# Optimization experiments

Measured on AMD Instinct MI355X. Metric: run time of the kernel, lower is better.

The kernel has to match this reference:

```python
import jax, jax.numpy as jnp
import numpy as np

UNITS = 2048
RHO = 0.99          # spectral_radius
LEAKY = 1.0         # leaky integration coefficient
INPUT_SCALING = 1.0
BIAS_SCALING = 1.0
B, T, D_IN = 32, 512, 128


def setup_inputs() -> dict:
    key = jax.random.key(0)
    k1, k2, k3 = jax.random.split(key, 3)
    inputs = jax.random.normal(k1, (B, T, D_IN), dtype=jnp.float32)
    h0 = jnp.zeros((B, UNITS), dtype=jnp.float32)
    # original uses deterministic +/-1 signs from pi digits; same structure: sign matrix * scaling
    kernel = jnp.where(jax.random.uniform(k2, (D_IN, UNITS)) >= 0.5, 1.0, -1.0).astype(jnp.float32) * INPUT_SCALING
    bias = jnp.where(jax.random.uniform(k3, (UNITS,)) >= 0.5, 1.0, -1.0).astype(jnp.float32) * BIAS_SCALING
    return {"inputs": inputs, "h0": h0, "kernel": kernel, "bias": bias}


def reference(inputs, h0, kernel, bias):
    # Precompute input projection for all timesteps: [B, T, U]
    u = jnp.einsum("btd,du->btu", inputs, kernel)

    def step(h, u_t):
        # prev @ recurrent_kernel == spectral_radius * cyclic shift of prev
        state_part = RHO * jnp.roll(h, 1, axis=-1)
        h_new = h * (1.0 - LEAKY) + jnp.tanh(u_t + bias + state_part) * LEAKY
        return h_new, h_new

    _, ys = jax.lax.scan(step, h0, jnp.swapaxes(u, 0, 1))  # scan over time
    return jnp.swapaxes(ys, 0, 1)  # [B, T, U]
```

## Files before the change

### kernel.cpp

```cpp
#include <hip/hip_runtime.h>
#include <hip/hip_bf16.h>

#define U_ 2048
#define T_ 512
#define K_ 128
#define B_ 32
#define RHO_ 0.99f
#define CPB 128
#define NTILES 9
#define NSLOTS 10

typedef __attribute__((ext_vector_type(8))) short short8;
typedef __attribute__((ext_vector_type(4))) float f32x4;

__device__ __forceinline__ float fast_tanh(float x) {
  float e = __builtin_amdgcn_exp2f(2.8853900817779268f * x);
  return 1.0f - 2.0f * __builtin_amdgcn_rcpf(e + 1.0f);
}

__device__ __forceinline__ unsigned short bf16_rne(float x) {
  unsigned int u = __float_as_uint(x);
  u += 0x7FFFu + ((u >> 16) & 1u);
  return (unsigned short)(u >> 16);
}

#define GLOAD_LDS16(gsrc, ldst)                                        \
  __builtin_amdgcn_global_load_lds(                                    \
      (const __attribute__((address_space(1))) void*)(gsrc),           \
      (__attribute__((address_space(3))) void*)(ldst), 16, 0, 0)

__global__ __launch_bounds__(256) void convert_a_kernel(
    const float* __restrict__ A, unsigned short* __restrict__ Ab) {
  const int gi = blockIdx.x * 256 + threadIdx.x;
  const int m = gi >> 5;
  const int kq = (gi & 31) << 2;
  const float4 v = *(const float4*)&A[(size_t)m * K_ + kq];
  ushort4 hi, lo;
  hi.x = bf16_rne(v.x); hi.y = bf16_rne(v.y); hi.z = bf16_rne(v.z); hi.w = bf16_rne(v.w);
  lo.x = bf16_rne(v.x - __uint_as_float((unsigned)hi.x << 16));
  lo.y = bf16_rne(v.y - __uint_as_float((unsigned)hi.y << 16));
  lo.z = bf16_rne(v.z - __uint_as_float((unsigned)hi.z << 16));
  lo.w = bf16_rne(v.w - __uint_as_float((unsigned)hi.w << 16));
  *(ushort4*)&Ab[(size_t)m * 256 + kq] = hi;
  *(ushort4*)&Ab[(size_t)m * 256 + 128 + kq] = lo;
}

__global__ __launch_bounds__(256) void convert_w_kernel(
    const float* __restrict__ W, unsigned short* __restrict__ Wbt) {
  const int gi = blockIdx.x * 256 + threadIdx.x;
  const int kq = gi >> 11;
  const int n = gi & 2047;
  const int k = kq << 2;
  ushort4 w;
  w.x = bf16_rne(W[(size_t)(k + 0) * U_ + n]);
  w.y = bf16_rne(W[(size_t)(k + 1) * U_ + n]);
  w.z = bf16_rne(W[(size_t)(k + 2) * U_ + n]);
  w.w = bf16_rne(W[(size_t)(k + 3) * U_ + n]);
  *(ushort4*)&Wbt[(size_t)n * 256 + k] = w;
  *(ushort4*)&Wbt[(size_t)n * 256 + 128 + k] = w;
}

__global__ __launch_bounds__(256, 2) void fused_gemm_scan4_kernel(
    const unsigned short* __restrict__ Ab, const unsigned short* __restrict__ Wbt,
    const float* __restrict__ bias, const float* __restrict__ h0,
    float* __restrict__ out) {
  __shared__ unsigned short Wl[NSLOTS * 2048];
  __shared__ unsigned short Al[2][4096];
  __shared__ float u_lds[2][16 * 146];
  const int tid = threadIdx.x;
  const int id = blockIdx.x + (blockIdx.y << 4);
  const int xcd = id & 7;
  const int wk = id >> 3;
  const int b = (xcd << 2) + (wk >> 4);
  const int bx = wk & 15;
  const int c0 = bx << 7;
  const int cbase = bx << 3;
  const int wave = tid >> 6;
  const int lane = tid & 63;
  const int r = lane & 15;
  const int q = lane >> 4;

  const int wrow = tid >> 4;
  const int wlg  = (tid & 15) ^ (wrow & 7);
  const int arow0 = tid >> 5;
  const int alg0  = (tid & 31) ^ (arow0 & 7);
  const int arow1 = 8 + arow0;
  const int alg1  = (tid & 31) ^ (arow1 & 7);

  const unsigned short* const aBase = Ab + (((size_t)b * T_) << 8);

  GLOAD_LDS16(aBase + (((size_t)arow0) << 8) + (alg0 << 3), &Al[0][tid << 3]);
  GLOAD_LDS16(aBase + (((size_t)arow1) << 8) + (alg1 << 3), &Al[0][(tid + 256) << 3]);
  #pragma unroll
  for (int j = 0; j < NTILES; ++j) {
    const int g = (cbase + j) & 127;
    GLOAD_LDS16(Wbt + (((size_t)((g << 4) + wrow)) << 8) + (wlg << 3),
                &Wl[(j << 11) + (tid << 3)]);
  }
  float bv[3], nbv[3];
  bv[0] = bias[(c0 + (wave << 4) + r) & (U_ - 1)];
  bv[1] = bias[(c0 + ((wave + 4) << 4) + r) & (U_ - 1)];
  bv[2] = (wave == 0) ? bias[(c0 + 128 + r) & (U_ - 1)] : 0.0f;
  float h = 0.0f;
  if (tid < CPB)
    h = h0[((size_t)b << 11) + ((c0 + tid + U_ - 1) & (U_ - 1))];

  __syncthreads();

  for (int it = 0; it < T_ / 16; ++it) {
    const int cur = it & 1;
    const int t0 = it << 4;

    if (it + 1 < T_ / 16) {
      GLOAD_LDS16(aBase + (((size_t)(t0 + 16 + arow0)) << 8) + (alg0 << 3),
                  &Al[cur ^ 1][tid << 3]);
      GLOAD_LDS16(aBase + (((size_t)(t0 + 16 + arow1)) << 8) + (alg1 << 3),
                  &Al[cur ^ 1][(tid + 256) << 3]);
      const int g = (cbase + it + NTILES) & 127;
      GLOAD_LDS16(Wbt + (((size_t)((g << 4) + wrow)) << 8) + (wlg << 3),
                  &Wl[(((it + NTILES) % NSLOTS) << 11) + (tid << 3)]);
      nbv[0] = bias[(c0 + t0 + 16 + (wave << 4) + r) & (U_ - 1)];
      nbv[1] = bias[(c0 + t0 + 16 + ((wave + 4) << 4) + r) & (U_ - 1)];
      if (wave == 0) nbv[2] = bias[(c0 + t0 + 16 + 128 + r) & (U_ - 1)];
    }

    short8 af[8];
    #pragma unroll
    for (int ks = 0; ks < 8; ++ks)
      af[ks] = *(const short8*)&Al[cur][(r << 8) + ((((ks << 2) + q) ^ (r & 7)) << 3)];

    #pragma unroll
    for (int u = 0; u < 3; ++u) {
      const int j = (u < 2) ? (wave + (u << 2)) : 8;
      if (u < 2 || wave == 0) {
        const int slot = (it + j) % NSLOTS;
        short8 bfk[4];
        #pragma unroll
        for (int ks = 0; ks < 4; ++ks)
          bfk[ks] = *(const short8*)&Wl[(slot << 11) + (r << 7) +
                                        ((((ks << 2) + q) ^ (r & 7)) << 3)];
        f32x4 acc = (f32x4){0.f, 0.f, 0.f, 0.f};
        #pragma unroll
        for (int ks = 0; ks < 8; ++ks)
          acc = __builtin_amdgcn_mfma_f32_16x16x32_bf16(af[ks], bfk[ks & 3], acc, 0, 0, 0);
        #pragma unroll
        for (int reg = 0; reg < 4; ++reg)
          u_lds[cur][((q << 2) + reg) * 146 + (j << 4) + r] = acc[reg] + bv[u];
      }
    }

    __syncthreads();

    if (tid < CPB) {
      float uv[16];
      #pragma unroll
      for (int tt = 0; tt < 16; ++tt)
        uv[tt] = u_lds[cur][tt * 146 + tid + tt];
      float* const orow = out + (((size_t)(b * T_ + t0)) << 11);
      #pragma unroll
      for (int tt = 0; tt < 16; ++tt) {
        h = fast_tanh(fmaf(RHO_, h, uv[tt]));
        __builtin_nontemporal_store(
            h, &orow[((size_t)tt << 11) + ((c0 + tid + t0 + tt) & (U_ - 1))]);
      }
    }
    bv[0] = nbv[0]; bv[1] = nbv[1]; bv[2] = nbv[2];
  }
}

__global__ __launch_bounds__(256) void ring_scan_kernel(
    float* __restrict__ buf, const float* __restrict__ h0) {
  const int b = blockIdx.y;
  const int c = (blockIdx.x << 8) + threadIdx.x;
  float* const base = buf + (size_t)b * (T_ * U_);
  float h = h0[((size_t)b << 11) + ((c + U_ - 1) & (U_ - 1))];
  float wA[8], wB[8];
  #pragma unroll
  for (int j = 0; j < 8; ++j)
    wA[j] = base[((size_t)j << 11) + ((c + j) & (U_ - 1))];
  for (int t0 = 0; t0 < T_; t0 += 16) {
    #pragma unroll
    for (int j = 0; j < 8; ++j) {
      const int t = t0 + 8 + j;
      wB[j] = base[((size_t)t << 11) + ((c + t) & (U_ - 1))];
    }
    #pragma unroll
    for (int j = 0; j < 8; ++j) {
      const int t = t0 + j;
      h = fast_tanh(fmaf(RHO_, h, wA[j]));
      base[((size_t)t << 11) + ((c + t) & (U_ - 1))] = h;
    }
    if (t0 + 16 < T_) {
      #pragma unroll
      for (int j = 0; j < 8; ++j) {
        const int t = t0 + 16 + j;
        wA[j] = base[((size_t)t << 11) + ((c + t) & (U_ - 1))];
      }
    }
    #pragma unroll
    for (int j = 0; j < 8; ++j) {
      const int t = t0 + 8 + j;
      h = fast_tanh(fmaf(RHO_, h, wB[j]));
      base[((size_t)t << 11) + ((c + t) & (U_ - 1))] = h;
    }
  }
}

__global__ __launch_bounds__(256, 4) void gemm_bias_kernel(
    const float* __restrict__ A, const float* __restrict__ W,
    const float* __restrict__ bias, float* __restrict__ out) {
  __shared__ float Asf[64][68];
  __shared__ float Bsf[64][64];
  const int tid = threadIdx.x;
  const int m0 = blockIdx.y << 6;
  const int n0 = blockIdx.x << 6;
  const int tx = tid & 15;
  const int ty = tid >> 4;
  float acc[4][4] = {};
  #pragma unroll
  for (int kb = 0; kb < 2; ++kb) {
    if (kb) __syncthreads();
    {
      const int c4 = tid & 15;
      const int r0 = tid >> 4;
      #pragma unroll
      for (int rr = 0; rr < 4; ++rr) {
        const int r = r0 + (rr << 4);
        const float4 v = *(const float4*)(A + (size_t)(m0 + r) * K_ + (kb << 6) + (c4 << 2));
        Asf[(c4 << 2) + 0][r] = v.x;
        Asf[(c4 << 2) + 1][r] = v.y;
        Asf[(c4 << 2) + 2][r] = v.z;
        Asf[(c4 << 2) + 3][r] = v.w;
      }
    }
    {
      const int c4 = tid & 15;
      const int r0 = tid >> 4;
      #pragma unroll
      for (int rr = 0; rr < 4; ++rr) {
        const int k = r0 + (rr << 4);
        *(float4*)&Bsf[k][c4 << 2] =
            *(const float4*)(W + (size_t)((kb << 6) + k) * U_ + n0 + (c4 << 2));
      }
    }
    __syncthreads();
    #pragma unroll 16
    for (int k = 0; k < 64; ++k) {
      const float4 a = *(const float4*)&Asf[k][ty << 2];
      const float4 b = *(const float4*)&Bsf[k][tx << 2];
      acc[0][0] = fmaf(a.x, b.x, acc[0][0]); acc[0][1] = fmaf(a.x, b.y, acc[0][1]);
      acc[0][2] = fmaf(a.x, b.z, acc[0][2]); acc[0][3] = fmaf(a.x, b.w, acc[0][3]);
      acc[1][0] = fmaf(a.y, b.x, acc[1][0]); acc[1][1] = fmaf(a.y, b.y, acc[1][1]);
      acc[1][2] = fmaf(a.y, b.z, acc[1][2]); acc[1][3] = fmaf(a.y, b.w, acc[1][3]);
      acc[2][0] = fmaf(a.z, b.x, acc[2][0]); acc[2][1] = fmaf(a.z, b.y, acc[2][1]);
      acc[2][2] = fmaf(a.z, b.z, acc[2][2]); acc[2][3] = fmaf(a.z, b.w, acc[2][3]);
      acc[3][0] = fmaf(a.w, b.x, acc[3][0]); acc[3][1] = fmaf(a.w, b.y, acc[3][1]);
      acc[3][2] = fmaf(a.w, b.z, acc[3][2]); acc[3][3] = fmaf(a.w, b.w, acc[3][3]);
    }
  }
  const float4 bv = *(const float4*)(bias + n0 + (tx << 2));
  #pragma unroll
  for (int i = 0; i < 4; ++i) {
    float4 o;
    o.x = acc[i][0] + bv.x; o.y = acc[i][1] + bv.y;
    o.z = acc[i][2] + bv.z; o.w = acc[i][3] + bv.w;
    *(float4*)(out + (size_t)(m0 + (ty << 2) + i) * U_ + n0 + (tx << 2)) = o;
  }
}

extern "C" void kernel_launch(void* const* d_in, const int* in_sizes, int n_in,
                              void* d_out, int out_size, void* d_ws, size_t ws_size,
                              hipStream_t stream) {
  const float* A    = (const float*)d_in[0];
  const float* h0   = (const float*)d_in[1];
  const float* W    = (const float*)d_in[2];
  const float* bias = (const float*)d_in[3];
  float* out = (float*)d_out;

  const size_t AB_BYTES = (size_t)B_ * T_ * 256 * 2;
  const size_t WB_BYTES = (size_t)U_ * 256 * 2;
  const size_t NEEDED = AB_BYTES + WB_BYTES;

  if (ws_size >= NEEDED) {
    unsigned short* Ab  = (unsigned short*)d_ws;
    unsigned short* Wbt = (unsigned short*)((char*)d_ws + AB_BYTES);

    convert_a_kernel<<<2048, 256, 0, stream>>>(A, Ab);
    convert_w_kernel<<<256, 256, 0, stream>>>(W, Wbt);
    dim3 fg(U_ / CPB, B_);
    fused_gemm_scan4_kernel<<<fg, 256, 0, stream>>>(Ab, Wbt, bias, h0, out);
  } else {
    dim3 gemm_grid(U_ / 64, (B_ * T_) / 64);
    gemm_bias_kernel<<<gemm_grid, 256, 0, stream>>>(A, W, bias, out);
    dim3 scan_grid(U_ / 256, B_);
    ring_scan_kernel<<<scan_grid, 256, 0, stream>>>(out, h0);
  }
}
```

Measured before the change: 192.7 us.

## Defer output stores by one iteration and move async loads to scan waves

The fused GEMM+scan kernel now buffers the 16 scan outputs in registers and stores them at the start of the next iteration, so the global stores overlap the MFMA work. All async global-to-LDS loads are issued by the first 128 threads, and the ninth-tile MFMA moves from wave 0 to wave 2. Together these spread the load across the waves that also run the scan. The block barrier becomes a hand-written waitcnt with vmcnt(16), so it no longer waits on outstanding stores. The tanh recurrence is also reformulated to fold RHO into the next step's FMA and shorten the serial dependency chain. The custom waitcnt depends on how the compiler orders memory operations and could be fragile.

```diff
diff --git a/kernel.cpp b/kernel.cpp
--- a/kernel.cpp
+++ b/kernel.cpp
@@ -12,11 +12,6 @@
 
 typedef __attribute__((ext_vector_type(8))) short short8;
 typedef __attribute__((ext_vector_type(4))) float f32x4;
-
-__device__ __forceinline__ float fast_tanh(float x) {
-  float e = __builtin_amdgcn_exp2f(2.8853900817779268f * x);
-  return 1.0f - 2.0f * __builtin_amdgcn_rcpf(e + 1.0f);
-}
 
 __device__ __forceinline__ unsigned short bf16_rne(float x) {
   unsigned int u = __float_as_uint(x);
@@ -60,7 +55,7 @@
   *(ushort4*)&Wbt[(size_t)n * 256 + 128 + k] = w;
 }
 
-__global__ __launch_bounds__(256, 2) void fused_gemm_scan4_kernel(
+__global__ __launch_bounds__(256, 2) void fused_gemm_scan5_kernel(
     const unsigned short* __restrict__ Ab, const unsigned short* __restrict__ Wbt,
     const float* __restrict__ bias, const float* __restrict__ h0,
     float* __restrict__ out) {
@@ -80,30 +75,36 @@
   const int r = lane & 15;
   const int q = lane >> 4;
 
-  const int wrow = tid >> 4;
-  const int wlg  = (tid & 15) ^ (wrow & 7);
-  const int arow0 = tid >> 5;
-  const int alg0  = (tid & 31) ^ (arow0 & 7);
-  const int arow1 = 8 + arow0;
-  const int alg1  = (tid & 31) ^ (arow1 & 7);
-
   const unsigned short* const aBase = Ab + (((size_t)b * T_) << 8);
 
-  GLOAD_LDS16(aBase + (((size_t)arow0) << 8) + (alg0 << 3), &Al[0][tid << 3]);
-  GLOAD_LDS16(aBase + (((size_t)arow1) << 8) + (alg1 << 3), &Al[0][(tid + 256) << 3]);
-  #pragma unroll
-  for (int j = 0; j < NTILES; ++j) {
-    const int g = (cbase + j) & 127;
-    GLOAD_LDS16(Wbt + (((size_t)((g << 4) + wrow)) << 8) + (wlg << 3),
-                &Wl[(j << 11) + (tid << 3)]);
+  if (tid < 128) {
+    #pragma unroll
+    for (int k = 0; k < 4; ++k) {
+      const int p = tid + (k << 7);
+      const int row = p >> 5, pg = p & 31;
+      GLOAD_LDS16(aBase + ((size_t)row << 8) + ((pg ^ (row & 7)) << 3),
+                  &Al[0][p << 3]);
+    }
+    #pragma unroll
+    for (int j = 0; j < NTILES; ++j) {
+      const int g = (cbase + j) & 127;
+      #pragma unroll
+      for (int k = 0; k < 2; ++k) {
+        const int p = tid + (k << 7);
+        const int row = p >> 4, pg = p & 15;
+        GLOAD_LDS16(Wbt + ((size_t)((g << 4) + row) << 8) + ((pg ^ (row & 7)) << 3),
+                    &Wl[(j << 11) + (p << 3)]);
+      }
+    }
   }
   float bv[3], nbv[3];
   bv[0] = bias[(c0 + (wave << 4) + r) & (U_ - 1)];
   bv[1] = bias[(c0 + ((wave + 4) << 4) + r) & (U_ - 1)];
-  bv[2] = (wave == 0) ? bias[(c0 + 128 + r) & (U_ - 1)] : 0.0f;
-  float h = 0.0f;
+  bv[2] = (wave == 2) ? bias[(c0 + 128 + r) & (U_ - 1)] : 0.0f;
+  float h_prev = 0.0f;
   if (tid < CPB)
-    h = h0[((size_t)b << 11) + ((c0 + tid + U_ - 1) & (U_ - 1))];
+    h_prev = h0[((size_t)b << 11) + ((c0 + tid + U_ - 1) & (U_ - 1))];
+  float hreg[16];
 
   __syncthreads();
 
@@ -111,17 +112,38 @@
     const int cur = it & 1;
     const int t0 = it << 4;
 
+    if (tid < 128 && it + 1 < T_ / 16) {
+      #pragma unroll
+      for (int k = 0; k < 4; ++k) {
+        const int p = tid + (k << 7);
+        const int row = p >> 5, pg = p & 31;
+        GLOAD_LDS16(aBase + ((size_t)(t0 + 16 + row) << 8) + ((pg ^ (row & 7)) << 3),
+                    &Al[cur ^ 1][p << 3]);
+      }
+      const int g = (cbase + it + NTILES) & 127;
+      const int snew = (it + NTILES) % NSLOTS;
+      #pragma unroll
+      for (int k = 0; k < 2; ++k) {
+        const int p = tid + (k << 7);
+        const int row = p >> 4, pg = p & 15;
+        GLOAD_LDS16(Wbt + ((size_t)((g << 4) + row) << 8) + ((pg ^ (row & 7)) << 3),
+                    &Wl[(snew << 11) + (p << 3)]);
+      }
+    }
     if (it + 1 < T_ / 16) {
-      GLOAD_LDS16(aBase + (((size_t)(t0 + 16 + arow0)) << 8) + (alg0 << 3),
-                  &Al[cur ^ 1][tid << 3]);
-      GLOAD_LDS16(aBase + (((size_t)(t0 + 16 + arow1)) << 8) + (alg1 << 3),
-                  &Al[cur ^ 1][(tid + 256) << 3]);
-      const int g = (cbase + it + NTILES) & 127;
-      GLOAD_LDS16(Wbt + (((size_t)((g << 4) + wrow)) << 8) + (wlg << 3),
-                  &Wl[(((it + NTILES) % NSLOTS) << 11) + (tid << 3)]);
       nbv[0] = bias[(c0 + t0 + 16 + (wave << 4) + r) & (U_ - 1)];
       nbv[1] = bias[(c0 + t0 + 16 + ((wave + 4) << 4) + r) & (U_ - 1)];
-      if (wave == 0) nbv[2] = bias[(c0 + t0 + 16 + 128 + r) & (U_ - 1)];
+      if (wave == 2) nbv[2] = bias[(c0 + t0 + 16 + 128 + r) & (U_ - 1)];
+    }
+    __builtin_amdgcn_sched_barrier(0);
+
+    if (tid < CPB && it > 0) {
+      const int t0p = t0 - 16;
+      float* const orow = out + (((size_t)(b * T_ + t0p)) << 11);
+      #pragma unroll
+      for (int tt = 0; tt < 16; ++tt)
+        __builtin_nontemporal_store(
+            hreg[tt], &orow[((size_t)tt << 11) + ((c0 + tid + t0p + tt) & (U_ - 1))]);
     }
 
     short8 af[8];
@@ -132,7 +154,7 @@
     #pragma unroll
     for (int u = 0; u < 3; ++u) {
       const int j = (u < 2) ? (wave + (u << 2)) : 8;
-      if (u < 2 || wave == 0) {
+      if (u < 2 || wave == 2) {
         const int slot = (it + j) % NSLOTS;
         short8 bfk[4];
         #pragma unroll
@@ -149,23 +171,40 @@
       }
     }
 
-    __syncthreads();
+    asm volatile("s_waitcnt vmcnt(16) lgkmcnt(0)\n\ts_barrier" ::: "memory");
+    __builtin_amdgcn_sched_barrier(0);
 
     if (tid < CPB) {
       float uv[16];
       #pragma unroll
       for (int tt = 0; tt < 16; ++tt)
         uv[tt] = u_lds[cur][tt * 146 + tid + tt];
-      float* const orow = out + (((size_t)(b * T_ + t0)) << 11);
+      float x = fmaf(RHO_, h_prev, uv[0]);
       #pragma unroll
       for (int tt = 0; tt < 16; ++tt) {
-        h = fast_tanh(fmaf(RHO_, h, uv[tt]));
-        __builtin_nontemporal_store(
-            h, &orow[((size_t)tt << 11) + ((c0 + tid + t0 + tt) & (U_ - 1))]);
-      }
+        float e = __builtin_amdgcn_exp2f(2.8853900817779268f * x);
+        float rc = __builtin_amdgcn_rcpf(e + 1.0f);
+        hreg[tt] = fmaf(-2.0f, rc, 1.0f);
+        if (tt < 15) x = fmaf(-2.0f * RHO_, rc, uv[tt + 1] + RHO_);
+      }
+      h_prev = hreg[15];
     }
     bv[0] = nbv[0]; bv[1] = nbv[1]; bv[2] = nbv[2];
   }
+
+  if (tid < CPB) {
+    const int t0p = T_ - 16;
+    float* const orow = out + (((size_t)(b * T_ + t0p)) << 11);
+    #pragma unroll
+    for (int tt = 0; tt < 16; ++tt)
+      __builtin_nontemporal_store(
+          hreg[tt], &orow[((size_t)tt << 11) + ((c0 + tid + t0p + tt) & (U_ - 1))]);
+  }
+}
+
+__device__ __forceinline__ float fast_tanh(float x) {
+  float e = __builtin_amdgcn_exp2f(2.8853900817779268f * x);
+  return 1.0f - 2.0f * __builtin_amdgcn_rcpf(e + 1.0f);
 }
 
 __global__ __launch_bounds__(256) void ring_scan_kernel(
@@ -288,7 +327,7 @@
     convert_a_kernel<<<2048, 256, 0, stream>>>(A, Ab);
     convert_w_kernel<<<256, 256, 0, stream>>>(W, Wbt);
     dim3 fg(U_ / CPB, B_);
-    fused_gemm_scan4_kernel<<<fg, 256, 0, stream>>>(Ab, Wbt, bias, h0, out);
+    fused_gemm_scan5_kernel<<<fg, 256, 0, stream>>>(Ab, Wbt, bias, h0, out);
   } else {
     dim3 gemm_grid(U_ / 64, (B_ * T_) / 64);
     gemm_bias_kernel<<<gemm_grid, 256, 0, stream>>>(A, W, bias, out);
```

Measured after the change: 193.4 us. No clear change (+0.4%).
